# Kernel optimization log

Measured on AMD Instinct MI355X. Metric: run time of the kernel, lower is better.

Reference implementation:

```python
import jax, jax.numpy as jnp
import numpy as np

B, N, H, W, P = 32, 6, 512, 512, 512
SCALE, ASPECT, MIN_PH = 0.5, 1.0, 60.0


def setup_inputs() -> dict:
    key = jax.random.key(0)
    k1, k2, k3, k4, k5, k6 = jax.random.split(key, 6)
    images = jax.random.normal(k1, (B, H, W, 3), jnp.float32)
    patch = jax.random.normal(k2, (P, P, 3), jnp.float32)
    # person bboxes (ymin, xmin, ymax, xmax) in pixels, fully inside the image
    hsz = jax.random.uniform(k3, (B, N), jnp.float32, 120.0, 400.0)
    wsz = jax.random.uniform(k4, (B, N), jnp.float32, 120.0, 400.0)
    ymin = jax.random.uniform(k5, (B, N), jnp.float32) * (H - hsz)
    xmin = jax.random.uniform(k6, (B, N), jnp.float32) * (W - wsz)
    boxes = jnp.stack([ymin, xmin, ymin + hsz, xmin + wsz], axis=-1)
    return {"images": images, "boxes": boxes, "patch": patch}


def _patch_boxes(boxes):
    # Patcher.create: derive (ymin_patch, xmin_patch, patch_h, patch_w) from each bbox
    ymin, xmin, ymax, xmax = (boxes[..., 0], boxes[..., 1], boxes[..., 2], boxes[..., 3])
    h = ymax - ymin
    w = xmax - xmin
    pw = h * SCALE
    ph = ASPECT * pw
    oy = ymin + h * 0.5
    ox = xmin + w * 0.5
    yp = jnp.maximum(oy - ph * 0.5, 0.0)
    xp = jnp.maximum(ox - pw * 0.5, 0.0)
    yp = jnp.where(yp + ph > H, H - ph, yp)
    xp = jnp.where(xp + pw > W, W - pw, xp)
    valid = ph > MIN_PH  # ragged filter -> mask
    return jnp.stack([yp, xp, ph, pw], axis=-1), valid


def _paste_one(img, patch, box, valid):
    # fused gather(resize bilinear, half-pixel centers) + scatter of the patch into img
    Pn = patch.shape[0]
    b = box.astype(jnp.int32)  # tf.cast truncation
    y0b, x0b, h, w = b[0], b[1], b[2], b[3]
    hf = jnp.maximum(h, 1).astype(jnp.float32)
    wf = jnp.maximum(w, 1).astype(jnp.float32)
    dy = jnp.arange(img.shape[0]) - y0b
    dx = jnp.arange(img.shape[1]) - x0b
    sy = jnp.clip((dy.astype(jnp.float32) + 0.5) * (Pn / hf) - 0.5, 0.0, Pn - 1.0)
    sx = jnp.clip((dx.astype(jnp.float32) + 0.5) * (Pn / wf) - 0.5, 0.0, Pn - 1.0)
    yl = jnp.floor(sy).astype(jnp.int32); yh = jnp.minimum(yl + 1, Pn - 1); wy = sy - yl
    xl = jnp.floor(sx).astype(jnp.int32); xh = jnp.minimum(xl + 1, Pn - 1); wx = sx - xl
    # separable bilinear: rows [H, P, 3] then cols -> [H, W, 3]
    rows = patch[yl] * (1.0 - wy)[:, None, None] + patch[yh] * wy[:, None, None]
    val = rows[:, xl] * (1.0 - wx)[None, :, None] + rows[:, xh] * wx[None, :, None]
    inside = ((dy >= 0) & (dy < h))[:, None] & ((dx >= 0) & (dx < w))[None, :] & valid
    return jnp.where(inside[..., None], val, img)


def reference(images, boxes, patch):
    pboxes, valid = _patch_boxes(boxes)
    def step(imgs, xs):
        bx, v = xs  # [B,4], [B]
        imgs = jax.vmap(lambda im, b_, v_: _paste_one(im, patch, b_, v_))(imgs, bx, v)
        return imgs, None
    # sequential over patches (later patches overwrite earlier, as in the tf while_loop)
    out, _ = jax.lax.scan(step, images, (jnp.transpose(pboxes, (1, 0, 2)), valid.T))
    return out
```

## Files before the change

### kernel.cpp

```cpp
#include <hip/hip_runtime.h>


#define Bn 32
#define Nn 6
#define Hh 512
#define Ww 512
#define Pp 512

__global__ __launch_bounds__(256) void patch_attack_kernel(
    const float* __restrict__ images,
    const float* __restrict__ boxes,
    const float* __restrict__ patch,
    float* __restrict__ out)
{
    const int pix = blockIdx.x * 256 + threadIdx.x;
    const int b   = blockIdx.x >> 10;
    const int rem = pix & (Hh * Ww - 1);
    const int y   = rem >> 9;
    const int x   = rem & (Ww - 1);

    const float* __restrict__ bx = boxes + (size_t)b * Nn * 4;

    float r0, r1, r2;
    bool covered = false;

    #pragma unroll
    for (int n = Nn - 1; n >= 0; --n) {
        const float ymin = bx[n * 4 + 0];
        const float xmin = bx[n * 4 + 1];
        const float ymax = bx[n * 4 + 2];
        const float xmax = bx[n * 4 + 3];
        const float h  = ymax - ymin;
        const float w  = xmax - xmin;
        const float pw = h * 0.5f;
        const float ph = 1.0f * pw;
        const float oy = ymin + h * 0.5f;
        const float ox = xmin + w * 0.5f;
        float yp = fmaxf(oy - ph * 0.5f, 0.0f);
        float xp = fmaxf(ox - pw * 0.5f, 0.0f);
        yp = (yp + ph > (float)Hh) ? ((float)Hh - ph) : yp;
        xp = (xp + pw > (float)Ww) ? ((float)Ww - pw) : xp;
        const bool valid = ph > 60.0f;

        const int y0b = (int)yp;
        const int x0b = (int)xp;
        const int hI  = (int)ph;
        const int wI  = (int)pw;
        const int dy  = y - y0b;
        const int dx  = x - x0b;

        if (valid && dy >= 0 && dy < hI && dx >= 0 && dx < wI) {
            const float hf = (float)(hI > 1 ? hI : 1);
            const float wf = (float)(wI > 1 ? wI : 1);
            float sy = ((float)dy + 0.5f) * ((float)Pp / hf) - 0.5f;
            float sx = ((float)dx + 0.5f) * ((float)Pp / wf) - 0.5f;
            sy = fminf(fmaxf(sy, 0.0f), (float)(Pp - 1));
            sx = fminf(fmaxf(sx, 0.0f), (float)(Pp - 1));
            const int   yl = (int)floorf(sy);
            const int   yh = (yl + 1 < Pp - 1) ? (yl + 1) : (Pp - 1);
            const float wy = sy - (float)yl;
            const int   xl = (int)floorf(sx);
            const int   xh = (xl + 1 < Pp - 1) ? (xl + 1) : (Pp - 1);
            const float wx = sx - (float)xl;

            const float* __restrict__ pll = patch + ((size_t)yl * Pp + xl) * 3;
            const float* __restrict__ plh = patch + ((size_t)yl * Pp + xh) * 3;
            const float* __restrict__ phl = patch + ((size_t)yh * Pp + xl) * 3;
            const float* __restrict__ phh = patch + ((size_t)yh * Pp + xh) * 3;
            const float omwy = 1.0f - wy;
            const float omwx = 1.0f - wx;
            r0 = (pll[0] * omwy + phl[0] * wy) * omwx + (plh[0] * omwy + phh[0] * wy) * wx;
            r1 = (pll[1] * omwy + phl[1] * wy) * omwx + (plh[1] * omwy + phh[1] * wy) * wx;
            r2 = (pll[2] * omwy + phl[2] * wy) * omwx + (plh[2] * omwy + phh[2] * wy) * wx;
            covered = true;
            break;
        }
    }

    if (!covered) {
        const float* __restrict__ ip = images + (size_t)pix * 3;
        r0 = ip[0];
        r1 = ip[1];
        r2 = ip[2];
    }

    float* __restrict__ op = out + (size_t)pix * 3;
    op[0] = r0;
    op[1] = r1;
    op[2] = r2;
}

extern "C" void kernel_launch(void* const* d_in, const int* in_sizes, int n_in,
                              void* d_out, int out_size, void* d_ws, size_t ws_size,
                              hipStream_t stream) {
    const float* images = (const float*)d_in[0];
    const float* boxes  = (const float*)d_in[1];
    const float* patch  = (const float*)d_in[2];
    float* out = (float*)d_out;

    const int total_pixels = Bn * Hh * Ww;
    const int block = 256;
    const int grid  = total_pixels / block;

    patch_attack_kernel<<<grid, block, 0, stream>>>(images, boxes, patch, out);
}
```

Before: 190.0 us.

## Process four pixels per thread with vectorized nontemporal IO and shared box params

Each thread now handles four consecutive pixels and reads and writes 48 bytes through three 16-byte nontemporal vector loads and stores. The per-box parameters are computed once per block into shared memory, and the row-dependent bilinear terms are hoisted out of the per-pixel loop. Each row does a cheap row-coverage check before any column work. The goal is to cut memory instruction count and redundant box math on this bandwidth-bound copy, at the cost of more registers and fewer threads.

```diff
diff --git a/kernel.cpp b/kernel.cpp
--- a/kernel.cpp
+++ b/kernel.cpp
@@ -1,11 +1,12 @@
 #include <hip/hip_runtime.h>
 
 
-#define Bn 32
 #define Nn 6
 #define Hh 512
 #define Ww 512
 #define Pp 512
+
+typedef float v4f __attribute__((ext_vector_type(4)));
 
 __global__ __launch_bounds__(256) void patch_attack_kernel(
     const float* __restrict__ images,
@@ -13,81 +14,117 @@
     const float* __restrict__ patch,
     float* __restrict__ out)
 {
-    const int pix = blockIdx.x * 256 + threadIdx.x;
-    const int b   = blockIdx.x >> 10;
-    const int rem = pix & (Hh * Ww - 1);
-    const int y   = rem >> 9;
-    const int x   = rem & (Ww - 1);
+    __shared__ int      s_y0[Nn], s_x0[Nn], s_h[Nn];
+    __shared__ unsigned s_w[Nn];
+    __shared__ float    s_sy[Nn], s_sx[Nn];
 
-    const float* __restrict__ bx = boxes + (size_t)b * Nn * 4;
+    const int b = blockIdx.x >> 8;
 
-    float r0, r1, r2;
-    bool covered = false;
-
-    #pragma unroll
-    for (int n = Nn - 1; n >= 0; --n) {
-        const float ymin = bx[n * 4 + 0];
-        const float xmin = bx[n * 4 + 1];
-        const float ymax = bx[n * 4 + 2];
-        const float xmax = bx[n * 4 + 3];
+    if (threadIdx.x < Nn) {
+        const int n = threadIdx.x;
+        const float* bx = boxes + ((size_t)b * Nn + n) * 4;
+        const float ymin = bx[0], xmin = bx[1], ymax = bx[2], xmax = bx[3];
         const float h  = ymax - ymin;
         const float w  = xmax - xmin;
         const float pw = h * 0.5f;
-        const float ph = 1.0f * pw;
+        const float ph = pw;
         const float oy = ymin + h * 0.5f;
         const float ox = xmin + w * 0.5f;
         float yp = fmaxf(oy - ph * 0.5f, 0.0f);
         float xp = fmaxf(ox - pw * 0.5f, 0.0f);
-        yp = (yp + ph > (float)Hh) ? ((float)Hh - ph) : yp;
-        xp = (xp + pw > (float)Ww) ? ((float)Ww - pw) : xp;
+        yp = (yp + ph > 512.0f) ? (512.0f - ph) : yp;
+        xp = (xp + pw > 512.0f) ? (512.0f - pw) : xp;
         const bool valid = ph > 60.0f;
+        const int hI = (int)ph;
+        const int wI = (int)pw;
+        s_y0[n] = (int)yp;
+        s_x0[n] = (int)xp;
+        s_h[n]  = valid ? hI : 0;
+        s_w[n]  = (unsigned)wI;
+        s_sy[n] = 512.0f / (float)(hI > 1 ? hI : 1);
+        s_sx[n] = 512.0f / (float)(wI > 1 ? wI : 1);
+    }
+    __syncthreads();
 
-        const int y0b = (int)yp;
-        const int x0b = (int)xp;
-        const int hI  = (int)ph;
-        const int wI  = (int)pw;
-        const int dy  = y - y0b;
-        const int dx  = x - x0b;
+    const int t    = blockIdx.x * 256 + threadIdx.x;
+    const int pix0 = t << 2;
+    const int rem  = pix0 & (Hh * Ww - 1);
+    const int y    = rem >> 9;
+    const int x0   = rem & (Ww - 1);
 
-        if (valid && dy >= 0 && dy < hI && dx >= 0 && dx < wI) {
-            const float hf = (float)(hI > 1 ? hI : 1);
-            const float wf = (float)(wI > 1 ? wI : 1);
-            float sy = ((float)dy + 0.5f) * ((float)Pp / hf) - 0.5f;
-            float sx = ((float)dx + 0.5f) * ((float)Pp / wf) - 0.5f;
-            sy = fminf(fmaxf(sy, 0.0f), (float)(Pp - 1));
-            sx = fminf(fmaxf(sx, 0.0f), (float)(Pp - 1));
-            const int   yl = (int)floorf(sy);
-            const int   yh = (yl + 1 < Pp - 1) ? (yl + 1) : (Pp - 1);
-            const float wy = sy - (float)yl;
-            const int   xl = (int)floorf(sx);
-            const int   xh = (xl + 1 < Pp - 1) ? (xl + 1) : (Pp - 1);
-            const float wx = sx - (float)xl;
+    unsigned wEff[Nn];
+    int   xo[Nn], offl[Nn], offh[Nn];
+    float wyv[Nn], omwy[Nn], sxs[Nn];
+    unsigned anyrow = 0;
+    #pragma unroll
+    for (int n = 0; n < Nn; ++n) {
+        const int dy = y - s_y0[n];
+        const bool rh = (unsigned)dy < (unsigned)s_h[n];
+        wEff[n] = rh ? s_w[n] : 0u;
+        anyrow |= wEff[n];
+        xo[n]  = s_x0[n];
+        sxs[n] = s_sx[n];
+        float sy = ((float)dy + 0.5f) * s_sy[n] - 0.5f;
+        sy = fminf(fmaxf(sy, 0.0f), 511.0f);
+        const int yl = (int)sy;
+        const int yh = (yl + 1 < 511) ? (yl + 1) : 511;
+        wyv[n]  = sy - (float)yl;
+        omwy[n] = 1.0f - wyv[n];
+        offl[n] = yl * (Pp * 3);
+        offh[n] = yh * (Pp * 3);
+    }
 
-            const float* __restrict__ pll = patch + ((size_t)yl * Pp + xl) * 3;
-            const float* __restrict__ plh = patch + ((size_t)yl * Pp + xh) * 3;
-            const float* __restrict__ phl = patch + ((size_t)yh * Pp + xl) * 3;
-            const float* __restrict__ phh = patch + ((size_t)yh * Pp + xh) * 3;
-            const float omwy = 1.0f - wy;
-            const float omwx = 1.0f - wx;
-            r0 = (pll[0] * omwy + phl[0] * wy) * omwx + (plh[0] * omwy + phh[0] * wy) * wx;
-            r1 = (pll[1] * omwy + phl[1] * wy) * omwx + (plh[1] * omwy + phh[1] * wy) * wx;
-            r2 = (pll[2] * omwy + phl[2] * wy) * omwx + (plh[2] * omwy + phh[2] * wy) * wx;
-            covered = true;
-            break;
+    float res[12];
+    unsigned covmask = 0;
+
+    if (anyrow) {
+        #pragma unroll
+        for (int j = 0; j < 4; ++j) {
+            const int x = x0 + j;
+            #pragma unroll
+            for (int n = Nn - 1; n >= 0; --n) {
+                const int dx = x - xo[n];
+                if ((unsigned)dx < wEff[n]) {
+                    float sx = ((float)dx + 0.5f) * sxs[n] - 0.5f;
+                    sx = fminf(fmaxf(sx, 0.0f), 511.0f);
+                    const int xl = (int)sx;
+                    const int xh = (xl + 1 < 511) ? (xl + 1) : 511;
+                    const float wx   = sx - (float)xl;
+                    const float omwx = 1.0f - wx;
+                    const float* __restrict__ rl = patch + offl[n];
+                    const float* __restrict__ rh_ = patch + offh[n];
+                    const int al = xl * 3, ah = xh * 3;
+                    res[j*3+0] = (rl[al+0]*omwy[n] + rh_[al+0]*wyv[n]) * omwx
+                               + (rl[ah+0]*omwy[n] + rh_[ah+0]*wyv[n]) * wx;
+                    res[j*3+1] = (rl[al+1]*omwy[n] + rh_[al+1]*wyv[n]) * omwx
+                               + (rl[ah+1]*omwy[n] + rh_[ah+1]*wyv[n]) * wx;
+                    res[j*3+2] = (rl[al+2]*omwy[n] + rh_[al+2]*wyv[n]) * omwx
+                               + (rl[ah+2]*omwy[n] + rh_[ah+2]*wyv[n]) * wx;
+                    covmask |= 1u << j;
+                    break;
+                }
+            }
         }
     }
 
-    if (!covered) {
-        const float* __restrict__ ip = images + (size_t)pix * 3;
-        r0 = ip[0];
-        r1 = ip[1];
-        r2 = ip[2];
+    if (covmask != 0xFu) {
+        const v4f* __restrict__ ip = (const v4f*)(images + (size_t)pix0 * 3);
+        const v4f i0 = __builtin_nontemporal_load(ip + 0);
+        const v4f i1 = __builtin_nontemporal_load(ip + 1);
+        const v4f i2 = __builtin_nontemporal_load(ip + 2);
+        if (!(covmask & 1u)) { res[0] = i0.x; res[1]  = i0.y; res[2]  = i0.z; }
+        if (!(covmask & 2u)) { res[3] = i0.w; res[4]  = i1.x; res[5]  = i1.y; }
+        if (!(covmask & 4u)) { res[6] = i1.z; res[7]  = i1.w; res[8]  = i2.x; }
+        if (!(covmask & 8u)) { res[9] = i2.y; res[10] = i2.z; res[11] = i2.w; }
     }
 
-    float* __restrict__ op = out + (size_t)pix * 3;
-    op[0] = r0;
-    op[1] = r1;
-    op[2] = r2;
+    v4f* __restrict__ op = (v4f*)(out + (size_t)pix0 * 3);
+    v4f o0 = { res[0], res[1], res[2],  res[3] };
+    v4f o1 = { res[4], res[5], res[6],  res[7] };
+    v4f o2 = { res[8], res[9], res[10], res[11] };
+    __builtin_nontemporal_store(o0, op + 0);
+    __builtin_nontemporal_store(o1, op + 1);
+    __builtin_nontemporal_store(o2, op + 2);
 }
 
 extern "C" void kernel_launch(void* const* d_in, const int* in_sizes, int n_in,
@@ -98,9 +135,8 @@
     const float* patch  = (const float*)d_in[2];
     float* out = (float*)d_out;
 
-    const int total_pixels = Bn * Hh * Ww;
-    const int block = 256;
-    const int grid  = total_pixels / block;
+    const int total_pixels = 32 * Hh * Ww;
+    const int grid = total_pixels / (256 * 4);
 
-    patch_attack_kernel<<<grid, block, 0, stream>>>(images, boxes, patch, out);
+    patch_attack_kernel<<<grid, 256, 0, stream>>>(images, boxes, patch, out);
 }
```

Measured after the change: 213.1 us. +12.1%, slower.
